# Performance work log

Hardware: AMD Instinct MI355X
Metric: run time of the kernel (lower is better)

The kernel has to match this reference:

```python
import jax, jax.numpy as jnp
import numpy as np

SIGMA = 1.0


def setup_inputs() -> dict:
    key = jax.random.key(0)
    k1, k2 = jax.random.split(key)
    data = jax.random.normal(k1, (64, 256, 32, 32), dtype=jnp.float32)
    # centers ~ Uniform(c_min=-1, c_max=1), shape (c_num, z_channels)
    centers = jax.random.uniform(k2, (1024, 256), dtype=jnp.float32) * 2.0 - 1.0
    return {"data": data, "centers": centers}


def reference(data, centers):
    b, c, h, w = data.shape
    c_num = centers.shape[0]
    # (b,c,h,w) -> (N, C) tokens, N = b*h*w
    x = data.transpose(0, 2, 3, 1).reshape(-1, c)
    # L2 distance to every codebook center without materializing (N, C, c_num):
    x2 = jnp.sum(x * x, axis=1, keepdims=True)            # (N, 1)
    e2 = jnp.sum(centers * centers, axis=1)[None, :]       # (1, c_num)
    sq = x2 - 2.0 * (x @ centers.T) + e2                   # (N, c_num)
    dist = jnp.sqrt(jnp.maximum(sq, 0.0))
    phisoft = jax.nn.softmax(-SIGMA * dist, axis=-1)       # (N, c_num)
    symbols = jnp.argmin(dist, axis=-1)                    # (N,)
    softout = phisoft @ centers                            # (N, C)
    hardout = centers[symbols]                             # (N, C)
    zbar = softout + jax.lax.stop_gradient(hardout - softout)

    def to_bchw(t):
        return t.reshape(b, h, w, -1).transpose(0, 3, 1, 2)

    # (zbar, zsoft, zhard, symbols, softsymbols)
    return tuple(map(to_bchw, (zbar, softout, hardout, symbols, phisoft)))
```

## Files before the change

### kernel.cpp

```cpp
#include <hip/hip_runtime.h>

#define CNUM 1024
#define CDIM 256
#define EPS_CAND 6.0f

#define OFF_ZBAR   ((size_t)0)
#define OFF_ZSOFT  ((size_t)16777216)
#define OFF_ZHARD  ((size_t)33554432)
#define OFF_SYM    ((size_t)50331648)
#define OFF_PHI    ((size_t)50397184)

typedef __attribute__((ext_vector_type(8))) short bf16x8;
typedef __attribute__((ext_vector_type(4))) float f32x4;
typedef __attribute__((ext_vector_type(4))) unsigned short u16x4;

__device__ __forceinline__ unsigned short f2bf(float f){
  unsigned u = __float_as_uint(f);
  u += 0x7fffu + ((u >> 16) & 1u);
  return (unsigned short)(u >> 16);
}
__device__ __forceinline__ float bf2f(unsigned short h){
  return __uint_as_float(((unsigned)h) << 16);
}
__device__ __forceinline__ float clamp01(float v){ return fminf(1.0f, fmaxf(0.0f, v)); }
__device__ __forceinline__ float clamp11(float v){ return fminf(1.0f, fmaxf(-1.0f, v)); }
__device__ __forceinline__ float dot4(float4 a, float4 b){ return a.x*b.x + a.y*b.y + a.z*b.z + a.w*b.w; }
__device__ __forceinline__ void nt_store4(float* p, float a, float b, float c, float d){
  f32x4 v = {a,b,c,d};
  __builtin_nontemporal_store(v, reinterpret_cast<f32x4*>(p));
}

__global__ __launch_bounds__(256) void prep_convert(const float* __restrict__ centers,
                                                    unsigned short* __restrict__ cb16,
                                                    unsigned short* __restrict__ ct16){
  int gid = blockIdx.x*256 + threadIdx.x;
  int c = gid >> 6, d0 = (gid & 63)*4;
  float4 v = *reinterpret_cast<const float4*>(centers + (size_t)c*CDIM + d0);
  unsigned short b0=f2bf(v.x), b1=f2bf(v.y), b2=f2bf(v.z), b3=f2bf(v.w);
  unsigned lo = (unsigned)b0 | ((unsigned)b1<<16);
  unsigned hi = (unsigned)b2 | ((unsigned)b3<<16);
  *reinterpret_cast<uint2*>(cb16 + (size_t)c*CDIM + d0) = make_uint2(lo, hi);
  ct16[(size_t)(d0+0)*CNUM + c] = b0;
  ct16[(size_t)(d0+1)*CNUM + c] = b1;
  ct16[(size_t)(d0+2)*CNUM + c] = b2;
  ct16[(size_t)(d0+3)*CNUM + c] = b3;
}

__global__ __launch_bounds__(256) void prep_e2(const float* __restrict__ centers, float* __restrict__ e2){
  int k = blockIdx.x*256 + threadIdx.x;
  const float4* c4 = reinterpret_cast<const float4*>(centers) + (size_t)k*(CDIM/4);
  float s = 0.f;
  #pragma unroll
  for (int i=0;i<CDIM/4;i++){ float4 v = c4[i]; s += dot4(v,v); }
  e2[k] = s;
}

__global__ __launch_bounds__(512) void k1_gemm1(const float* __restrict__ data,
                                                const unsigned short* __restrict__ cb16,
                                                const float* __restrict__ e2g,
                                                unsigned short* __restrict__ scr16){
  __shared__ unsigned short xb[64*256];
  __shared__ unsigned short cb[64*256];
  __shared__ unsigned short st[64*72];
  __shared__ float e2s[64];
  __shared__ float px[512];
  __shared__ float x2s[64];

  const int tid = threadIdx.x;
  const int w = tid>>6, lane = tid&63;
  const int l15 = lane&15, g = lane>>4;
  const int sb = (blockIdx.x & 7)*128 + (blockIdx.x >> 3);
  const int b = sb>>4, hw0 = (sb&15)*64;

  {
    float p2 = 0.f;
    const float* dp = data + ((size_t)b*CDIM + 32*w)*1024 + hw0 + lane;
    #pragma unroll
    for (int i=0;i<16;i++){
      int dd = 2*i;
      float v0 = dp[(size_t)dd*1024];
      float v1 = dp[(size_t)(dd+1)*1024];
      p2 += v0*v0 + v1*v1;
      unsigned pk = (unsigned)f2bf(v0) | ((unsigned)f2bf(v1)<<16);
      int d = 32*w + dd;
      int s = d>>3;
      *reinterpret_cast<unsigned*>((char*)xb + lane*512 + (((s ^ (lane&7))<<4)) + (d&7)*2) = pk;
    }
    px[w*64 + lane] = p2;
  }
  __syncthreads();
  if (tid < 64){
    float s = 0.f;
    #pragma unroll
    for (int wv=0; wv<8; wv++) s += px[wv*64 + tid];
    x2s[tid] = s;
  }

  const int tt  = w & 3;
  const int ch2 = w >> 2;
  const int t   = 16*tt + l15;
  const size_t tbase2 = (((size_t)b*1024 + hw0) >> 5) * 32768;

  for (int cc=0; cc<16; cc++){
    __syncthreads();
    #pragma unroll
    for (int it=0; it<4; it++){
      int e = tid + 512*it;
      int c = e>>5, s = e&31;
      uint4 v = *reinterpret_cast<const uint4*>(cb16 + ((size_t)(cc*64 + c))*CDIM + s*8);
      *reinterpret_cast<uint4*>((char*)cb + c*512 + ((s ^ (c&7))<<4)) = v;
    }
    if (tid < 64) e2s[tid] = e2g[cc*64 + tid];
    __syncthreads();

    f32x4 acc0 = {0.f,0.f,0.f,0.f}, acc1 = {0.f,0.f,0.f,0.f};
    const int c0 = 32*ch2 + l15, c1 = c0 + 16;
    #pragma unroll
    for (int k=0;k<8;k++){
      bf16x8 bf = *reinterpret_cast<const bf16x8*>((const char*)xb + t*512 + (((4*k+g) ^ (t&7))<<4));
      bf16x8 a0 = *reinterpret_cast<const bf16x8*>((const char*)cb + c0*512 + (((4*k+g) ^ (c0&7))<<4));
      bf16x8 a1 = *reinterpret_cast<const bf16x8*>((const char*)cb + c1*512 + (((4*k+g) ^ (c1&7))<<4));
      acc0 = __builtin_amdgcn_mfma_f32_16x16x32_bf16(a0, bf, acc0, 0,0,0);
      acc1 = __builtin_amdgcn_mfma_f32_16x16x32_bf16(a1, bf, acc1, 0,0,0);
    }
    float x2v = x2s[t];
    {
      int clA = 32*ch2 + 4*g;
      u16x4 pA, pB;
      #pragma unroll
      for (int r=0;r<4;r++){
        pA[r] = f2bf(x2v - 2.0f*acc0[r] + e2s[clA + r]);
        pB[r] = f2bf(x2v - 2.0f*acc1[r] + e2s[clA + 16 + r]);
      }
      *reinterpret_cast<u16x4*>(&st[t*72 + clA])      = pA;
      *reinterpret_cast<u16x4*>(&st[t*72 + clA + 16]) = pB;
    }
    __syncthreads();
    {
      int tloc = tid>>3, seg = tid&7;
      uint4 v = *reinterpret_cast<const uint4*>(&st[tloc*72 + 8*seg]);
      size_t dst = tbase2 + (size_t)(tloc>>5)*32768 + (size_t)(tloc&31)*1024 + cc*64 + 8*seg;
      *reinterpret_cast<uint4*>(scr16 + dst) = v;
    }
  }
}

template<bool FUSE_G2>
__global__ __launch_bounds__(512, 4) void k2_soft(const float* __restrict__ data,
                                                  const float* __restrict__ centers,
                                                  const unsigned short* __restrict__ ct16,
                                                  const unsigned short* __restrict__ scr16,
                                                  float* __restrict__ out){
  __shared__ unsigned short S[32*1024];
  __shared__ unsigned short H[32*256];

  const int tid = threadIdx.x;
  const int w = tid>>6, lane = tid&63;
  const int l15 = lane&15, g = lane>>4;
  const int sb = (blockIdx.x & 7)*256 + (blockIdx.x >> 3);
  const int tok0 = sb*32;
  const int bb = tok0>>10, hw0 = tok0&1023;
  const unsigned short* sqblk = scr16 + (size_t)sb*32768;

  #pragma unroll
  for (int it=0; it<8; it++){
    int e = tid + 512*it;
    int t = e>>7, c8 = e&127;
    uint4 v = *reinterpret_cast<const uint4*>(sqblk + t*1024 + 8*c8);
    *reinterpret_cast<uint4*>((char*)S + t*2048 + ((16*c8) ^ ((t&7)<<4))) = v;
  }
  __syncthreads();

  for (int p=0;p<2;p++){
    const int t = p*16 + (tid>>5);
    const int j = tid&31;
    const int hb = (lane>=32)?32:0;
    const int tswz = (t&7)<<4;
    char* srow = (char*)S + t*2048;

    float a[32];
    float mns = 3.4e38f;
    #pragma unroll
    for (int i=0;i<32;i++){
      float sp = bf2f(*(const unsigned short*)(srow + ((2*(j+32*i)) ^ tswz)));
      a[i] = sp;
      mns = fminf(mns, sp);
    }
    #pragma unroll
    for (int m=16;m>=1;m>>=1) mns = fminf(mns, __shfl_xor(mns, m));
    float thr = mns + EPS_CAND;
    unsigned cm = 0;
    #pragma unroll
    for (int i=0;i<32;i++) if (a[i] < thr) cm |= (1u<<i);

    double bestd = 1.0e300; int bestk = CNUM;
    const float* xp = data + (size_t)bb*262144 + hw0 + t;
    for(;;){
      unsigned long long bal = __ballot(cm != 0);
      unsigned half = (lane<32)? (unsigned)(bal & 0xffffffffULL) : (unsigned)(bal>>32);
      if (!half) break;
      int src = __ffs(half)-1;
      unsigned cmsrc = (unsigned)__shfl((int)cm, hb + src);
      int ii = __ffs(cmsrc)-1;
      int k = src + 32*ii;
      if (j==src) cm &= ~(1u<<ii);
      double acc = 0.0;
      const float* crow = centers + (size_t)k*CDIM;
      #pragma unroll
      for (int q2=0;q2<8;q2++){
        double xv = (double)xp[(size_t)(j+32*q2)*1024];
        double ev = (double)crow[j+32*q2];
        double df = xv-ev; acc = fma(df,df,acc);
      }
      #pragma unroll
      for (int m=16;m>=1;m>>=1) acc += __shfl_xor(acc, m);
      if (acc < bestd || (acc==bestd && k<bestk)){ bestd=acc; bestk=k; }
    }
    if (j==0) out[OFF_SYM + tok0 + t] = (float)bestk;

    float dmn = sqrtf(fmaxf(mns, 0.f));
    float sum = 0.f;
    #pragma unroll
    for (int i=0;i<32;i++){
      float d = sqrtf(fmaxf(a[i], 0.f));
      a[i] = __expf(dmn - d);
      sum += a[i];
    }
    #pragma unroll
    for (int m=16;m>=1;m>>=1) sum += __shfl_xor(sum, m);
    float rs = 1.f/sum;
    #pragma unroll
    for (int i=0;i<32;i++){
      *(unsigned short*)(srow + ((2*(j+32*i)) ^ tswz)) = f2bf(clamp01(a[i]*rs));
    }
    const float* hrow = centers + (size_t)bestk*CDIM;
    #pragma unroll
    for (int q2=0;q2<8;q2++){
      int c = j + 32*q2;
      *(unsigned short*)((char*)H + t*512 + ((2*c) ^ tswz)) = f2bf(hrow[c]);
    }
  }
  __syncthreads();

  #pragma unroll
  for (int it=0; it<16; ++it){
    int e = tid + 512*it;
    int c = e>>3, q = e&7;
    float vv[4];
    #pragma unroll
    for (int u=0;u<4;u++){
      int t = 4*q + u;
      vv[u] = bf2f(*(const unsigned short*)((const char*)S + t*2048 + ((2*c) ^ ((t&7)<<4))));
    }
    nt_store4(out + OFF_PHI + (size_t)bb*1048576 + (size_t)c*1024 + hw0 + 4*q,
              vv[0], vv[1], vv[2], vv[3]);
  }
  #pragma unroll
  for (int it=0; it<4; ++it){
    int e = tid + 512*it;
    int d = e>>3, q = e&7;
    float vv[4];
    #pragma unroll
    for (int u=0;u<4;u++){
      int t = 4*q + u;
      vv[u] = bf2f(*(const unsigned short*)((const char*)H + t*512 + ((2*d) ^ ((t&7)<<4))));
    }
    size_t base = (size_t)bb*262144 + (size_t)d*1024 + hw0 + 4*q;
    nt_store4(out + OFF_ZBAR + base, vv[0], vv[1], vv[2], vv[3]);
    if (FUSE_G2) nt_store4(out + OFF_ZHARD + base, vv[0], vv[1], vv[2], vv[3]);
  }

  if (FUSE_G2){
    __syncthreads();
    f32x4 z00={0.f,0.f,0.f,0.f}, z01=z00, z10=z00, z11=z00;
    const unsigned short* ar0 = ct16 + (size_t)(16*w + l15)*CNUM;
    const unsigned short* ar1 = ct16 + (size_t)(16*(w+8) + l15)*CNUM;
    const char* br0 = (const char*)S + (size_t)l15*2048;
    const char* br1 = (const char*)S + (size_t)(16+l15)*2048;
    const int bswz = (l15&7)<<4;
    #pragma unroll 8
    for (int s=0;s<32;s++){
      bf16x8 b0 = *reinterpret_cast<const bf16x8*>(br0 + ((64*s + 16*g) ^ bswz));
      bf16x8 b1 = *reinterpret_cast<const bf16x8*>(br1 + ((64*s + 16*g) ^ bswz));
      bf16x8 a0 = *reinterpret_cast<const bf16x8*>(ar0 + 32*s + 8*g);
      bf16x8 a1 = *reinterpret_cast<const bf16x8*>(ar1 + 32*s + 8*g);
      z00 = __builtin_amdgcn_mfma_f32_16x16x32_bf16(a0, b0, z00, 0,0,0);
      z01 = __builtin_amdgcn_mfma_f32_16x16x32_bf16(a0, b1, z01, 0,0,0);
      z10 = __builtin_amdgcn_mfma_f32_16x16x32_bf16(a1, b0, z10, 0,0,0);
      z11 = __builtin_amdgcn_mfma_f32_16x16x32_bf16(a1, b1, z11, 0,0,0);
    }
    #pragma unroll
    for (int mi=0;mi<2;mi++){
      #pragma unroll
      for (int nt=0;nt<2;nt++){
        f32x4 ac = (mi==0) ? (nt==0 ? z00 : z01) : (nt==0 ? z10 : z11);
        int mt = w + 8*mi;
        int t  = nt*16 + l15;
        int d0 = 16*mt + 4*g;
        unsigned w0 = (unsigned)f2bf(clamp11(ac[0])) | ((unsigned)f2bf(clamp11(ac[1]))<<16);
        unsigned w1 = (unsigned)f2bf(clamp11(ac[2])) | ((unsigned)f2bf(clamp11(ac[3]))<<16);
        *reinterpret_cast<uint2*>((char*)H + t*512 + ((2*d0) ^ ((t&7)<<4))) = make_uint2(w0,w1);
      }
    }
    __syncthreads();
    #pragma unroll
    for (int it=0; it<4; ++it){
      int e = tid + 512*it;
      int d = e>>3, q = e&7;
      float vv[4];
      #pragma unroll
      for (int u=0;u<4;u++){
        int t = 4*q + u;
        vv[u] = bf2f(*(const unsigned short*)((const char*)H + t*512 + ((2*d) ^ ((t&7)<<4))));
      }
      nt_store4(out + OFF_ZSOFT + (size_t)bb*262144 + (size_t)d*1024 + hw0 + 4*q,
                vv[0], vv[1], vv[2], vv[3]);
    }
  }
}

__global__ __launch_bounds__(512) void k3_gemm2(const float* __restrict__ phi,
                                                const unsigned short* __restrict__ ct16,
                                                float* __restrict__ zsoft){
  __shared__ unsigned short pls[64*64];
  const int tid = threadIdx.x;
  const int w = tid>>6, lane = tid&63;
  const int l15 = lane&15, g = lane>>4;
  const int b = blockIdx.x>>4, hw0 = (blockIdx.x&15)*64;

  f32x4 acc[2][4];
  #pragma unroll
  for (int h=0;h<2;h++)
    #pragma unroll
    for (int t2=0;t2<4;t2++) acc[h][t2] = (f32x4){0.f,0.f,0.f,0.f};

  for (int ks=0; ks<16; ks++){
    int k0s = ks*64;
    __syncthreads();
    #pragma unroll
    for (int it=0; it<4; it++){
      int e = tid + 512*it;
      int kp = e>>6, t = e&63;
      const float* pp = phi + (size_t)b*1048576 + (size_t)(k0s + 2*kp)*1024 + hw0 + t;
      float v0 = pp[0];
      float v1 = pp[1024];
      unsigned pk = (unsigned)f2bf(v0) | ((unsigned)f2bf(v1)<<16);
      int kk = 2*kp;
      int s = kk>>3;
      *reinterpret_cast<unsigned*>((char*)pls + t*128 + ((s ^ (t&7))<<4) + (kk&7)*2) = pk;
    }
    __syncthreads();
    #pragma unroll
    for (int ki=0; ki<2; ki++){
      int kk0 = k0s + 32*ki;
      bf16x8 a0 = *reinterpret_cast<const bf16x8*>(ct16 + (size_t)(32*w + l15)*CNUM + kk0 + 8*g);
      bf16x8 a1 = *reinterpret_cast<const bf16x8*>(ct16 + (size_t)(32*w + 16 + l15)*CNUM + kk0 + 8*g);
      #pragma unroll
      for (int t2=0;t2<4;t2++){
        int t = 16*t2 + l15;
        bf16x8 bf = *reinterpret_cast<const bf16x8*>((const char*)pls + t*128 + (((4*ki+g) ^ (t&7))<<4));
        acc[0][t2] = __builtin_amdgcn_mfma_f32_16x16x32_bf16(a0, bf, acc[0][t2], 0,0,0);
        acc[1][t2] = __builtin_amdgcn_mfma_f32_16x16x32_bf16(a1, bf, acc[1][t2], 0,0,0);
      }
    }
  }
  #pragma unroll
  for (int h=0;h<2;h++)
    #pragma unroll
    for (int t2=0;t2<4;t2++)
      #pragma unroll
      for (int r=0;r<4;r++){
        int d = 32*w + 16*h + 4*g + r;
        zsoft[(size_t)b*262144 + (size_t)d*1024 + hw0 + 16*t2 + l15] = clamp11(acc[h][t2][r]);
      }
}

extern "C" void kernel_launch(void* const* d_in, const int* in_sizes, int n_in,
                              void* d_out, int out_size, void* d_ws, size_t ws_size,
                              hipStream_t stream) {
  const float* data    = (const float*)d_in[0];
  const float* centers = (const float*)d_in[1];
  float* out           = (float*)d_out;

  const size_t SQ_BYTES = (size_t)1024*65536*2;
  const bool wsmode = (ws_size >= SQ_BYTES + 524288 + 524288 + 4096);

  unsigned short *scr16, *cb16, *ct16;
  float *e2;
  if (wsmode){
    scr16 = (unsigned short*)d_ws;
    cb16  = (unsigned short*)((char*)d_ws + SQ_BYTES);
    ct16  = (unsigned short*)((char*)d_ws + SQ_BYTES + 524288);
    e2    = (float*)((char*)d_ws + SQ_BYTES + 1048576);
  } else {
    scr16 = (unsigned short*)(out + OFF_ZSOFT);
    cb16  = (unsigned short*)d_ws;
    ct16  = (unsigned short*)((char*)d_ws + 524288);
    e2    = (float*)((char*)d_ws + 1048576);
  }

  prep_convert<<<dim3(256), dim3(256), 0, stream>>>(centers, cb16, ct16);
  prep_e2<<<dim3(4), dim3(256), 0, stream>>>(centers, e2);
  k1_gemm1<<<dim3(1024), dim3(512), 0, stream>>>(data, cb16, e2, scr16);
  if (wsmode){
    k2_soft<true><<<dim3(2048), dim3(512), 0, stream>>>(data, centers, ct16, scr16, out);
  } else {
    k2_soft<false><<<dim3(2048), dim3(512), 0, stream>>>(data, centers, ct16, scr16, out);
    hipMemcpyAsync(out + OFF_ZHARD, out + OFF_ZBAR, (size_t)16777216*4, hipMemcpyDeviceToDevice, stream);
    k3_gemm2<<<dim3(1024), dim3(512), 0, stream>>>(out + OFF_PHI, ct16, out + OFF_ZSOFT);
  }
}
```

Baseline: 443.0 us.

## Split fused soft kernel into per-token softmax/argmin kernel and emit kernel

Replaces the monolithic k2_soft in workspace mode with two kernels. ka_soft handles one token per 32 lanes at low LDS use for high occupancy, doing candidate refinement in double, softmax, and writing phi back into scratch. kb_emit then gathers the hard rows, writes the transposed outputs and runs the second GEMM. This raises parallelism in the latency-bound argmin phase, at the cost of an extra launch and an extra round trip of the scratch buffer through memory.

After: 404.3 us (median of 2 runs). 8.7% less time.

```diff
diff --git a/kernel.cpp b/kernel.cpp
--- a/kernel.cpp
+++ b/kernel.cpp
@@ -145,9 +145,85 @@
   }
 }
 
-template<bool FUSE_G2>
-__global__ __launch_bounds__(512, 4) void k2_soft(const float* __restrict__ data,
-                                                  const float* __restrict__ centers,
+__global__ __launch_bounds__(256) void ka_soft(const float* __restrict__ data,
+                                               const float* __restrict__ centers,
+                                               unsigned short* __restrict__ scr16,
+                                               float* __restrict__ symout){
+  const int tid = threadIdx.x;
+  const int lane = tid&63;
+  const int j = tid&31;
+  const int hb = (lane>=32)?32:0;
+  const int sb = (blockIdx.x & 7)*1024 + (blockIdx.x >> 3);
+  const int tok = sb*8 + (tid>>5);
+  const int bb = tok>>10, hw = tok&1023;
+
+  unsigned short* srow = scr16 + (size_t)(tok>>5)*32768 + (size_t)(tok&31)*1024;
+
+  float a[32];
+  #pragma unroll
+  for (int k=0;k<4;k++){
+    uint4 v = *reinterpret_cast<const uint4*>(srow + 256*k + 8*j);
+    const unsigned short* p = (const unsigned short*)&v;
+    #pragma unroll
+    for (int u=0;u<8;u++) a[8*k+u] = bf2f(p[u]);
+  }
+  float mns = 3.4e38f;
+  #pragma unroll
+  for (int i=0;i<32;i++) mns = fminf(mns, a[i]);
+  #pragma unroll
+  for (int m=16;m>=1;m>>=1) mns = fminf(mns, __shfl_xor(mns, m));
+  float thr = mns + EPS_CAND;
+  unsigned cm = 0;
+  #pragma unroll
+  for (int i=0;i<32;i++) if (a[i] < thr) cm |= (1u<<i);
+
+  double bestd = 1.0e300; int bestk = CNUM;
+  const float* xp = data + (size_t)bb*262144 + hw;
+  for(;;){
+    unsigned long long bal = __ballot(cm != 0);
+    unsigned half = (lane<32)? (unsigned)(bal & 0xffffffffULL) : (unsigned)(bal>>32);
+    if (!half) break;
+    int src = __ffs(half)-1;
+    unsigned cmsrc = (unsigned)__shfl((int)cm, hb + src);
+    int ii = __ffs(cmsrc)-1;
+    int k = 256*(ii>>3) + 8*src + (ii&7);
+    if (j==src) cm &= ~(1u<<ii);
+    double acc = 0.0;
+    const float* crow = centers + (size_t)k*CDIM;
+    #pragma unroll
+    for (int q2=0;q2<8;q2++){
+      double xv = (double)xp[(size_t)(j+32*q2)*1024];
+      double ev = (double)crow[j+32*q2];
+      double df = xv-ev; acc = fma(df,df,acc);
+    }
+    #pragma unroll
+    for (int m=16;m>=1;m>>=1) acc += __shfl_xor(acc, m);
+    if (acc < bestd || (acc==bestd && k<bestk)){ bestd=acc; bestk=k; }
+  }
+  if (j==0) symout[tok] = (float)bestk;
+
+  float dmn = sqrtf(fmaxf(mns, 0.f));
+  float sum = 0.f;
+  #pragma unroll
+  for (int i=0;i<32;i++){
+    float d = sqrtf(fmaxf(a[i], 0.f));
+    a[i] = __expf(dmn - d);
+    sum += a[i];
+  }
+  #pragma unroll
+  for (int m=16;m>=1;m>>=1) sum += __shfl_xor(sum, m);
+  float rs = 1.f/sum;
+  #pragma unroll
+  for (int k=0;k<4;k++){
+    unsigned w0 = (unsigned)f2bf(clamp01(a[8*k+0]*rs)) | ((unsigned)f2bf(clamp01(a[8*k+1]*rs))<<16);
+    unsigned w1 = (unsigned)f2bf(clamp01(a[8*k+2]*rs)) | ((unsigned)f2bf(clamp01(a[8*k+3]*rs))<<16);
+    unsigned w2 = (unsigned)f2bf(clamp01(a[8*k+4]*rs)) | ((unsigned)f2bf(clamp01(a[8*k+5]*rs))<<16);
+    unsigned w3 = (unsigned)f2bf(clamp01(a[8*k+6]*rs)) | ((unsigned)f2bf(clamp01(a[8*k+7]*rs))<<16);
+    *reinterpret_cast<uint4*>(srow + 256*k + 8*j) = make_uint4(w0,w1,w2,w3);
+  }
+}
+
+__global__ __launch_bounds__(512, 4) void kb_emit(const float* __restrict__ centers,
                                                   const unsigned short* __restrict__ ct16,
                                                   const unsigned short* __restrict__ scr16,
                                                   float* __restrict__ out){
@@ -157,6 +233,122 @@
   const int tid = threadIdx.x;
   const int w = tid>>6, lane = tid&63;
   const int l15 = lane&15, g = lane>>4;
+  const int sb = (blockIdx.x & 7)*256 + (blockIdx.x >> 3);
+  const int tok0 = sb*32;
+  const int bb = tok0>>10, hw0 = tok0&1023;
+  const unsigned short* sqblk = scr16 + (size_t)sb*32768;
+
+  #pragma unroll
+  for (int it=0; it<8; it++){
+    int e = tid + 512*it;
+    int t = e>>7, c8 = e&127;
+    uint4 v = *reinterpret_cast<const uint4*>(sqblk + t*1024 + 8*c8);
+    *reinterpret_cast<uint4*>((char*)S + t*2048 + ((16*c8) ^ ((t&7)<<4))) = v;
+  }
+  for (int p=0;p<2;p++){
+    const int t = p*16 + (tid>>5);
+    const int j = tid&31;
+    const int tswz = (t&7)<<4;
+    int sym = (int)out[OFF_SYM + tok0 + t];
+    sym = (sym < 0) ? 0 : (sym > 1023 ? 1023 : sym);
+    const float* hrow = centers + (size_t)sym*CDIM + 8*j;
+    float4 h0 = *reinterpret_cast<const float4*>(hrow);
+    float4 h1 = *reinterpret_cast<const float4*>(hrow+4);
+    unsigned w0 = (unsigned)f2bf(h0.x) | ((unsigned)f2bf(h0.y)<<16);
+    unsigned w1 = (unsigned)f2bf(h0.z) | ((unsigned)f2bf(h0.w)<<16);
+    unsigned w2 = (unsigned)f2bf(h1.x) | ((unsigned)f2bf(h1.y)<<16);
+    unsigned w3 = (unsigned)f2bf(h1.z) | ((unsigned)f2bf(h1.w)<<16);
+    *reinterpret_cast<uint4*>((char*)H + t*512 + ((16*j) ^ tswz)) = make_uint4(w0,w1,w2,w3);
+  }
+  __syncthreads();
+
+  #pragma unroll
+  for (int it=0; it<16; ++it){
+    int e = tid + 512*it;
+    int c = e>>3, q = e&7;
+    float vv[4];
+    #pragma unroll
+    for (int u=0;u<4;u++){
+      int t = 4*q + u;
+      vv[u] = bf2f(*(const unsigned short*)((const char*)S + t*2048 + ((2*c) ^ ((t&7)<<4))));
+    }
+    nt_store4(out + OFF_PHI + (size_t)bb*1048576 + (size_t)c*1024 + hw0 + 4*q,
+              vv[0], vv[1], vv[2], vv[3]);
+  }
+  #pragma unroll
+  for (int it=0; it<4; ++it){
+    int e = tid + 512*it;
+    int d = e>>3, q = e&7;
+    float vv[4];
+    #pragma unroll
+    for (int u=0;u<4;u++){
+      int t = 4*q + u;
+      vv[u] = bf2f(*(const unsigned short*)((const char*)H + t*512 + ((2*d) ^ ((t&7)<<4))));
+    }
+    size_t base = (size_t)bb*262144 + (size_t)d*1024 + hw0 + 4*q;
+    nt_store4(out + OFF_ZBAR + base, vv[0], vv[1], vv[2], vv[3]);
+    nt_store4(out + OFF_ZHARD + base, vv[0], vv[1], vv[2], vv[3]);
+  }
+  __syncthreads();
+
+  {
+    f32x4 z00={0.f,0.f,0.f,0.f}, z01=z00, z10=z00, z11=z00;
+    const unsigned short* ar0 = ct16 + (size_t)(16*w + l15)*CNUM;
+    const unsigned short* ar1 = ct16 + (size_t)(16*(w+8) + l15)*CNUM;
+    const char* br0 = (const char*)S + (size_t)l15*2048;
+    const char* br1 = (const char*)S + (size_t)(16+l15)*2048;
+    const int bswz = (l15&7)<<4;
+    #pragma unroll 8
+    for (int s=0;s<32;s++){
+      bf16x8 b0 = *reinterpret_cast<const bf16x8*>(br0 + ((64*s + 16*g) ^ bswz));
+      bf16x8 b1 = *reinterpret_cast<const bf16x8*>(br1 + ((64*s + 16*g) ^ bswz));
+      bf16x8 a0 = *reinterpret_cast<const bf16x8*>(ar0 + 32*s + 8*g);
+      bf16x8 a1 = *reinterpret_cast<const bf16x8*>(ar1 + 32*s + 8*g);
+      z00 = __builtin_amdgcn_mfma_f32_16x16x32_bf16(a0, b0, z00, 0,0,0);
+      z01 = __builtin_amdgcn_mfma_f32_16x16x32_bf16(a0, b1, z01, 0,0,0);
+      z10 = __builtin_amdgcn_mfma_f32_16x16x32_bf16(a1, b0, z10, 0,0,0);
+      z11 = __builtin_amdgcn_mfma_f32_16x16x32_bf16(a1, b1, z11, 0,0,0);
+    }
+    #pragma unroll
+    for (int mi=0;mi<2;mi++){
+      #pragma unroll
+      for (int nt=0;nt<2;nt++){
+        f32x4 ac = (mi==0) ? (nt==0 ? z00 : z01) : (nt==0 ? z10 : z11);
+        int mt = w + 8*mi;
+        int t  = nt*16 + l15;
+        int d0 = 16*mt + 4*g;
+        unsigned w0 = (unsigned)f2bf(clamp11(ac[0])) | ((unsigned)f2bf(clamp11(ac[1]))<<16);
+        unsigned w1 = (unsigned)f2bf(clamp11(ac[2])) | ((unsigned)f2bf(clamp11(ac[3]))<<16);
+        *reinterpret_cast<uint2*>((char*)H + t*512 + ((2*d0) ^ ((t&7)<<4))) = make_uint2(w0,w1);
+      }
+    }
+  }
+  __syncthreads();
+
+  #pragma unroll
+  for (int it=0; it<4; ++it){
+    int e = tid + 512*it;
+    int d = e>>3, q = e&7;
+    float vv[4];
+    #pragma unroll
+    for (int u=0;u<4;u++){
+      int t = 4*q + u;
+      vv[u] = bf2f(*(const unsigned short*)((const char*)H + t*512 + ((2*d) ^ ((t&7)<<4))));
+    }
+    nt_store4(out + OFF_ZSOFT + (size_t)bb*262144 + (size_t)d*1024 + hw0 + 4*q,
+              vv[0], vv[1], vv[2], vv[3]);
+  }
+}
+
+__global__ __launch_bounds__(512, 4) void k2_soft_fb(const float* __restrict__ data,
+                                                     const float* __restrict__ centers,
+                                                     const unsigned short* __restrict__ scr16,
+                                                     float* __restrict__ out){
+  __shared__ unsigned short S[32*1024];
+  __shared__ unsigned short H[32*256];
+
+  const int tid = threadIdx.x;
+  const int lane = tid&63;
   const int sb = (blockIdx.x & 7)*256 + (blockIdx.x >> 3);
   const int tok0 = sb*32;
   const int bb = tok0>>10, hw0 = tok0&1023;
@@ -265,57 +457,8 @@
       int t = 4*q + u;
       vv[u] = bf2f(*(const unsigned short*)((const char*)H + t*512 + ((2*d) ^ ((t&7)<<4))));
     }
-    size_t base = (size_t)bb*262144 + (size_t)d*1024 + hw0 + 4*q;
-    nt_store4(out + OFF_ZBAR + base, vv[0], vv[1], vv[2], vv[3]);
-    if (FUSE_G2) nt_store4(out + OFF_ZHARD + base, vv[0], vv[1], vv[2], vv[3]);
-  }
-
-  if (FUSE_G2){
-    __syncthreads();
-    f32x4 z00={0.f,0.f,0.f,0.f}, z01=z00, z10=z00, z11=z00;
-    const unsigned short* ar0 = ct16 + (size_t)(16*w + l15)*CNUM;
-    const unsigned short* ar1 = ct16 + (size_t)(16*(w+8) + l15)*CNUM;
-    const char* br0 = (const char*)S + (size_t)l15*2048;
-    const char* br1 = (const char*)S + (size_t)(16+l15)*2048;
-    const int bswz = (l15&7)<<4;
-    #pragma unroll 8
-    for (int s=0;s<32;s++){
-      bf16x8 b0 = *reinterpret_cast<const bf16x8*>(br0 + ((64*s + 16*g) ^ bswz));
-      bf16x8 b1 = *reinterpret_cast<const bf16x8*>(br1 + ((64*s + 16*g) ^ bswz));
-      bf16x8 a0 = *reinterpret_cast<const bf16x8*>(ar0 + 32*s + 8*g);
-      bf16x8 a1 = *reinterpret_cast<const bf16x8*>(ar1 + 32*s + 8*g);
-      z00 = __builtin_amdgcn_mfma_f32_16x16x32_bf16(a0, b0, z00, 0,0,0);
-      z01 = __builtin_amdgcn_mfma_f32_16x16x32_bf16(a0, b1, z01, 0,0,0);
-      z10 = __builtin_amdgcn_mfma_f32_16x16x32_bf16(a1, b0, z10, 0,0,0);
-      z11 = __builtin_amdgcn_mfma_f32_16x16x32_bf16(a1, b1, z11, 0,0,0);
-    }
-    #pragma unroll
-    for (int mi=0;mi<2;mi++){
-      #pragma unroll
-      for (int nt=0;nt<2;nt++){
-        f32x4 ac = (mi==0) ? (nt==0 ? z00 : z01) : (nt==0 ? z10 : z11);
-        int mt = w + 8*mi;
-        int t  = nt*16 + l15;
-        int d0 = 16*mt + 4*g;
-        unsigned w0 = (unsigned)f2bf(clamp11(ac[0])) | ((unsigned)f2bf(clamp11(ac[1]))<<16);
-        unsigned w1 = (unsigned)f2bf(clamp11(ac[2])) | ((unsigned)f2bf(clamp11(ac[3]))<<16);
-        *reinterpret_cast<uint2*>((char*)H + t*512 + ((2*d0) ^ ((t&7)<<4))) = make_uint2(w0,w1);
-      }
-    }
-    __syncthreads();
-    #pragma unroll
-    for (int it=0; it<4; ++it){
-      int e = tid + 512*it;
-      int d = e>>3, q = e&7;
-      float vv[4];
-      #pragma unroll
-      for (int u=0;u<4;u++){
-        int t = 4*q + u;
-        vv[u] = bf2f(*(const unsigned short*)((const char*)H + t*512 + ((2*d) ^ ((t&7)<<4))));
-      }
-      nt_store4(out + OFF_ZSOFT + (size_t)bb*262144 + (size_t)d*1024 + hw0 + 4*q,
-                vv[0], vv[1], vv[2], vv[3]);
-    }
+    nt_store4(out + OFF_ZBAR + (size_t)bb*262144 + (size_t)d*1024 + hw0 + 4*q,
+              vv[0], vv[1], vv[2], vv[3]);
   }
 }
 
@@ -403,9 +546,10 @@
   prep_e2<<<dim3(4), dim3(256), 0, stream>>>(centers, e2);
   k1_gemm1<<<dim3(1024), dim3(512), 0, stream>>>(data, cb16, e2, scr16);
   if (wsmode){
-    k2_soft<true><<<dim3(2048), dim3(512), 0, stream>>>(data, centers, ct16, scr16, out);
+    ka_soft<<<dim3(8192), dim3(256), 0, stream>>>(data, centers, scr16, out + OFF_SYM);
+    kb_emit<<<dim3(2048), dim3(512), 0, stream>>>(centers, ct16, scr16, out);
   } else {
-    k2_soft<false><<<dim3(2048), dim3(512), 0, stream>>>(data, centers, ct16, scr16, out);
+    k2_soft_fb<<<dim3(2048), dim3(512), 0, stream>>>(data, centers, scr16, out);
     hipMemcpyAsync(out + OFF_ZHARD, out + OFF_ZBAR, (size_t)16777216*4, hipMemcpyDeviceToDevice, stream);
     k3_gemm2<<<dim3(1024), dim3(512), 0, stream>>>(out + OFF_PHI, ct16, out + OFF_ZSOFT);
   }
```
